# Kernel tuning notes

Hardware: AMD Instinct MI355X
Metric: run time of the kernel (lower is better)

The kernel has to match this reference:

```python
import jax, jax.numpy as jnp
import numpy as np

EPS = 1e-5  # torch LayerNorm default


def _ln(x, w, b):
    m = jnp.mean(x, axis=-1, keepdims=True)
    v = jnp.mean((x - m) ** 2, axis=-1, keepdims=True)
    return (x - m) / jnp.sqrt(v + EPS) * w + b


def _conv1x1(x, w, b):
    # x: [B,C,H,W], w: [O,C], b: [O]
    return jnp.einsum('bchw,oc->bohw', x, w) + b[None, :, None, None]


def setup_inputs() -> dict:
    key = jax.random.key(0)
    ks = jax.random.split(key, 5)
    B, Cin, H, W = 8, 384, 64, 64
    D, N = 128, 512
    s = lambda k, shape, scale=0.02: jax.random.normal(k, shape, jnp.float32) * scale
    return {
        'x': jax.random.normal(ks[0], (B, Cin, H, W), jnp.float32),
        'DR': jax.random.normal(ks[1], (N, D), jnp.float32),
        'conv_in_w': s(ks[2], (D, Cin)),
        'conv_in_b': jnp.zeros((D,), jnp.float32),
        'sem_w': s(ks[3], (D, D)),
        'sem_b': jnp.zeros((D,), jnp.float32),
        'norm1_w': jnp.ones((D,), jnp.float32),
        'norm1_b': jnp.zeros((D,), jnp.float32),
        'norm2_w': jnp.ones((D,), jnp.float32),
        'norm2_b': jnp.zeros((D,), jnp.float32),
        'conv_out_w': s(ks[4], (Cin, D)),
        'conv_out_b': jnp.zeros((Cin,), jnp.float32),
    }


def reference(x, DR, conv_in_w, conv_in_b, sem_w, sem_b, norm1_w, norm1_b,
              norm2_w, norm2_b, conv_out_w, conv_out_b):
    B, _, H, W = x.shape
    N = DR.shape[0]
    x_align = _conv1x1(x, conv_in_w, conv_in_b)                      # [B,D,H,W]
    x_sem = _conv1x1(x_align, sem_w, sem_b)                          # semantic_extra (1x1 conv)
    x_sem = x_sem.transpose(0, 2, 3, 1).reshape(B, H * W, -1)        # [B,HW,D]
    x_sem = _ln(x_sem, norm1_w, norm1_b)
    dr = _ln(DR, norm2_w, norm2_b).T                                 # [D,N] (same for all batches)
    # NOTE: original applies norm_1 TWICE for the numerator (faithful quirk)
    c_u = jnp.einsum('bld,dn->bln', _ln(x_sem, norm1_w, norm1_b), dr)  # [B,HW,N]
    c_d_l = jnp.sqrt(jnp.sum(x_sem ** 2, axis=-1, keepdims=True))      # [B,HW,1]
    c_d_r = jnp.sqrt(jnp.sum(dr ** 2, axis=0, keepdims=True))[None]    # [1,1,N]
    sim = c_u / (c_d_l * c_d_r)
    sim_soft = jax.nn.softmax(sim, axis=-1)                          # [B,HW,N]
    sim2d = sim_soft.transpose(0, 2, 1).reshape(B, N, H, W)
    degrad = jnp.einsum('bln,dn->bdl', sim_soft, dr).reshape(B, -1, H, W)  # [B,D,H,W]
    # pow-mask with per-batch min-max normalization
    mask_v = jnp.max(sim2d ** 3, axis=1, keepdims=True)              # [B,1,H,W]
    mn = jnp.min(mask_v.reshape(B, -1), axis=1).reshape(B, 1, 1, 1)
    mx = jnp.max(mask_v.reshape(B, -1), axis=1).reshape(B, 1, 1, 1)
    mask_v = 1.0 - (mask_v - mn) / (mx - mn)
    # topk row selection (torch fancy indexing gives [B,B,K,N]; squeeze(1) is a no-op for B>1)
    max_values = jnp.max(sim_soft, axis=2)                           # [B,HW]
    K = (H * W) // 50
    _, top_idx = jax.lax.top_k(max_values, K)                        # [B,K]
    results = jnp.take(sim_soft, top_idx, axis=1)                    # [B,B,K,N]
    out_img = _conv1x1(degrad, conv_out_w, conv_out_b)               # [B,Cin,H,W]
    return (mask_v, out_img, results)
```

## Files before the change

### kernel.cpp

```cpp
#include <hip/hip_runtime.h>
#include <cstdint>

#define EPS 1e-5f
#define BB   8
#define CIN  384
#define HWs  4096
#define LT   32768
#define DD   128
#define NN   512
#define TOPK 81

typedef short short8 __attribute__((ext_vector_type(8)));
typedef float f32x4  __attribute__((ext_vector_type(4)));

__device__ __forceinline__ unsigned short f2bf(float x) {
  unsigned u = __float_as_uint(x);
  u += 0x7fffu + ((u >> 16) & 1u);
  return (unsigned short)(u >> 16);
}
__device__ __forceinline__ float bf2f(unsigned u16) {
  return __uint_as_float(u16 << 16);
}
__device__ __forceinline__ void put_frag(unsigned short* buf, int tile, int rc, int k, float v) {
  int ks = k >> 5, g = (k >> 3) & 3, j = k & 7;
  int basehw = ((tile * 4 + ks) * 2) * 512 + (g * 16 + rc) * 8 + j;
  unsigned short hi = f2bf(v);
  buf[basehw] = hi;
  buf[basehw + 512] = f2bf(v - bf2f(hi));
}

__global__ __launch_bounds__(64) void k_dr(const float* __restrict__ DR,
    const float* __restrict__ w2, const float* __restrict__ b2,
    const float* __restrict__ w1, const float* __restrict__ b1,
    unsigned short* __restrict__ drwF, unsigned short* __restrict__ drlnF,
    float* __restrict__ t2, float* __restrict__ rcr) {
  int n = blockIdx.x;
  int lane = threadIdx.x;
  const float* row = DR + n * DD;
  float x0 = row[lane], x1 = row[lane + 64];
  float s = x0 + x1, sq = x0 * x0 + x1 * x1;
  #pragma unroll
  for (int o = 32; o; o >>= 1) { s += __shfl_xor(s, o); sq += __shfl_xor(sq, o); }
  float m = s * (1.f / 128.f);
  float v = sq * (1.f / 128.f) - m * m;
  float inv = rsqrtf(v + EPS);
  float y0 = (x0 - m) * inv * w2[lane] + b2[lane];
  float y1 = (x1 - m) * inv * w2[lane + 64] + b2[lane + 64];
  int nt = n >> 4, cc = n & 15;
  put_frag(drwF, nt, cc, lane, y0 * w1[lane]);
  put_frag(drwF, nt, cc, lane + 64, y1 * w1[lane + 64]);
  int ks = n >> 5, gB = (n >> 3) & 3, j = n & 7;
  {
    int d = lane;
    unsigned short hi = f2bf(y0);
    int base = (((d >> 4) * 16 + ks) * 2) * 512 + (gB * 16 + (d & 15)) * 8 + j;
    drlnF[base] = hi;
    drlnF[base + 512] = f2bf(y0 - bf2f(hi));
  }
  {
    int d = lane + 64;
    unsigned short hi = f2bf(y1);
    int base = (((d >> 4) * 16 + ks) * 2) * 512 + (gB * 16 + (d & 15)) * 8 + j;
    drlnF[base] = hi;
    drlnF[base + 512] = f2bf(y1 - bf2f(hi));
  }
  float pt2 = y0 * b1[lane] + y1 * b1[lane + 64];
  float pss = y0 * y0 + y1 * y1;
  #pragma unroll
  for (int o = 32; o; o >>= 1) { pt2 += __shfl_xor(pt2, o); pss += __shfl_xor(pss, o); }
  if (lane == 0) { t2[n] = pt2; rcr[n] = rsqrtf(pss); }
}

__global__ __launch_bounds__(256) void k_bprep(const float* __restrict__ src,
                                               unsigned short* __restrict__ dst,
                                               int K) {
  int rt = blockIdx.x, kb = blockIdx.y;
  int t = threadIdx.x, m = t >> 4, kg = t & 15;
  int k0 = kb * 128 + kg * 8;
  const float* s = src + (size_t)(rt * 16 + m) * K + k0;
  float4 f0 = *(const float4*)s;
  float4 f1 = *(const float4*)(s + 4);
  float vs[8] = {f0.x, f0.y, f0.z, f0.w, f1.x, f1.y, f1.z, f1.w};
  short8 hi, lo;
  #pragma unroll
  for (int j = 0; j < 8; ++j) {
    unsigned short h = f2bf(vs[j]);
    hi[j] = (short)h;
    lo[j] = (short)f2bf(vs[j] - bf2f(h));
  }
  int nkt = K >> 5;
  int ks = k0 >> 5, g = (k0 >> 3) & 3;
  short8* D8 = (short8*)dst;
  int base = ((rt * nkt + ks) * 2) * 64 + g * 16 + m;
  D8[base] = hi;
  D8[base + 64] = lo;
}

__global__ __launch_bounds__(256) void k_convsem(const float* __restrict__ x,
    const unsigned short* __restrict__ WinF, const float* __restrict__ bin,
    const unsigned short* __restrict__ semWF, const float* __restrict__ sb,
    const float* __restrict__ w1, const float* __restrict__ b1,
    unsigned short* __restrict__ ApF, float* __restrict__ rclv) {
  __shared__ unsigned int shbuf[32 * 132];
  __shared__ float sredS[32][4], sredQ[32][4];
  __shared__ float rowM[32], rowI[32];
  int t = threadIdx.x;
  int w = t >> 6, lane = t & 63, m = lane & 15, g = lane >> 4;
  int l0 = blockIdx.x * 32;
  int b = l0 >> 12, hw0 = l0 & 4095;
  const float* xb = x + (size_t)b * CIN * HWs + hw0;
  const short8* B8 = (const short8*)WinF;
  int chs = t & 31, hwo = (t >> 5) * 4;
  const float* xs = xb + (size_t)chs * HWs + hwo;
  f32x4 acc[2][2];
  #pragma unroll
  for (int lt = 0; lt < 2; ++lt)
    #pragma unroll
    for (int j2 = 0; j2 < 2; ++j2) acc[lt][j2] = (f32x4){0.f, 0.f, 0.f, 0.f};
  float4 u = *(const float4*)xs;
  for (int ks = 0; ks < 12; ++ks) {
    {
      float vv[4] = {u.x, u.y, u.z, u.w};
      #pragma unroll
      for (int i = 0; i < 4; ++i) {
        unsigned short h = f2bf(vv[i]);
        unsigned short lo = f2bf(vv[i] - bf2f(h));
        shbuf[(hwo + i) * 36 + chs] = (unsigned)h | ((unsigned)lo << 16);
      }
    }
    __syncthreads();
    if (ks < 11) u = *(const float4*)(xs + (size_t)((ks + 1) * 32) * HWs);
    short8 ah[2], al[2];
    #pragma unroll
    for (int lt = 0; lt < 2; ++lt) {
      const unsigned* src = &shbuf[(lt * 16 + m) * 36 + g * 8];
      uint4 p0 = *(const uint4*)(src);
      uint4 p1 = *(const uint4*)(src + 4);
      unsigned uu[8] = {p0.x, p0.y, p0.z, p0.w, p1.x, p1.y, p1.z, p1.w};
      unsigned* ahp = (unsigned*)&ah[lt];
      unsigned* alp = (unsigned*)&al[lt];
      #pragma unroll
      for (int jj = 0; jj < 4; ++jj) {
        unsigned e0 = uu[2 * jj], e1 = uu[2 * jj + 1];
        ahp[jj] = (e0 & 0xffffu) | (e1 << 16);
        alp[jj] = (e0 >> 16) | (e1 & 0xffff0000u);
      }
    }
    #pragma unroll
    for (int j2 = 0; j2 < 2; ++j2) {
      int dt = w * 2 + j2;
      short8 bh = B8[((dt * 12 + ks) * 2 + 0) * 64 + lane];
      short8 bl = B8[((dt * 12 + ks) * 2 + 1) * 64 + lane];
      #pragma unroll
      for (int lt = 0; lt < 2; ++lt) {
        acc[lt][j2] = __builtin_amdgcn_mfma_f32_16x16x32_bf16(ah[lt], bh, acc[lt][j2], 0, 0, 0);
        acc[lt][j2] = __builtin_amdgcn_mfma_f32_16x16x32_bf16(ah[lt], bl, acc[lt][j2], 0, 0, 0);
        acc[lt][j2] = __builtin_amdgcn_mfma_f32_16x16x32_bf16(al[lt], bh, acc[lt][j2], 0, 0, 0);
      }
    }
    __syncthreads();
  }
  {
    float bia[2] = {bin[w * 32 + m], bin[w * 32 + 16 + m]};
    #pragma unroll
    for (int lt = 0; lt < 2; ++lt)
      #pragma unroll
      for (int j2 = 0; j2 < 2; ++j2)
        #pragma unroll
        for (int r = 0; r < 4; ++r) {
          float v = acc[lt][j2][r] + bia[j2];
          unsigned short h = f2bf(v);
          unsigned short lo = f2bf(v - bf2f(h));
          shbuf[(lt * 16 + g * 4 + r) * 132 + (w * 2 + j2) * 16 + m] =
              (unsigned)h | ((unsigned)lo << 16);
        }
  }
  __syncthreads();
  const short8* S8 = (const short8*)semWF;
  f32x4 acc2[2][2];
  #pragma unroll
  for (int lt = 0; lt < 2; ++lt)
    #pragma unroll
    for (int j2 = 0; j2 < 2; ++j2) acc2[lt][j2] = (f32x4){0.f, 0.f, 0.f, 0.f};
  #pragma unroll
  for (int ks2 = 0; ks2 < 4; ++ks2) {
    short8 ah2[2], al2[2];
    #pragma unroll
    for (int lt = 0; lt < 2; ++lt) {
      const unsigned* src = &shbuf[(lt * 16 + m) * 132 + ks2 * 32 + g * 8];
      uint4 p0 = *(const uint4*)(src);
      uint4 p1 = *(const uint4*)(src + 4);
      unsigned uu[8] = {p0.x, p0.y, p0.z, p0.w, p1.x, p1.y, p1.z, p1.w};
      unsigned* ahp = (unsigned*)&ah2[lt];
      unsigned* alp = (unsigned*)&al2[lt];
      #pragma unroll
      for (int jj = 0; jj < 4; ++jj) {
        unsigned e0 = uu[2 * jj], e1 = uu[2 * jj + 1];
        ahp[jj] = (e0 & 0xffffu) | (e1 << 16);
        alp[jj] = (e0 >> 16) | (e1 & 0xffff0000u);
      }
    }
    #pragma unroll
    for (int j2 = 0; j2 < 2; ++j2) {
      int dt = w * 2 + j2;
      short8 bh = S8[((dt * 4 + ks2) * 2 + 0) * 64 + lane];
      short8 bl = S8[((dt * 4 + ks2) * 2 + 1) * 64 + lane];
      #pragma unroll
      for (int lt = 0; lt < 2; ++lt) {
        acc2[lt][j2] = __builtin_amdgcn_mfma_f32_16x16x32_bf16(ah2[lt], bh, acc2[lt][j2], 0, 0, 0);
        acc2[lt][j2] = __builtin_amdgcn_mfma_f32_16x16x32_bf16(ah2[lt], bl, acc2[lt][j2], 0, 0, 0);
        acc2[lt][j2] = __builtin_amdgcn_mfma_f32_16x16x32_bf16(al2[lt], bh, acc2[lt][j2], 0, 0, 0);
      }
    }
  }
  {
    float bia2[2] = {sb[w * 32 + m], sb[w * 32 + 16 + m]};
    #pragma unroll
    for (int lt = 0; lt < 2; ++lt)
      #pragma unroll
      for (int j2 = 0; j2 < 2; ++j2)
        #pragma unroll
        for (int r = 0; r < 4; ++r) acc2[lt][j2][r] += bia2[j2];
  }
  float s1[2][4], q1[2][4];
  #pragma unroll
  for (int lt = 0; lt < 2; ++lt)
    #pragma unroll
    for (int r = 0; r < 4; ++r) {
      float a = acc2[lt][0][r], b2v = acc2[lt][1][r];
      s1[lt][r] = a + b2v;
      q1[lt][r] = a * a + b2v * b2v;
    }
  #pragma unroll
  for (int o = 1; o < 16; o <<= 1)
    #pragma unroll
    for (int lt = 0; lt < 2; ++lt)
      #pragma unroll
      for (int r = 0; r < 4; ++r) {
        s1[lt][r] += __shfl_xor(s1[lt][r], o);
        q1[lt][r] += __shfl_xor(q1[lt][r], o);
      }
  if (m == 0) {
    #pragma unroll
    for (int lt = 0; lt < 2; ++lt)
      #pragma unroll
      for (int r = 0; r < 4; ++r) {
        sredS[lt * 16 + g * 4 + r][w] = s1[lt][r];
        sredQ[lt * 16 + g * 4 + r][w] = q1[lt][r];
      }
  }
  __syncthreads();
  if (t < 32) {
    float S = sredS[t][0] + sredS[t][1] + sredS[t][2] + sredS[t][3];
    float Q = sredQ[t][0] + sredQ[t][1] + sredQ[t][2] + sredQ[t][3];
    float mu = S * (1.f / 128.f);
    float var = Q * (1.f / 128.f) - mu * mu;
    rowM[t] = mu;
    rowI[t] = rsqrtf(var + EPS);
  }
  __syncthreads();
  float w1v[2] = {w1[w * 32 + m], w1[w * 32 + 16 + m]};
  float b1v[2] = {b1[w * 32 + m], b1[w * 32 + 16 + m]};
  #pragma unroll
  for (int lt = 0; lt < 2; ++lt)
    #pragma unroll
    for (int r = 0; r < 4; ++r) {
      float mu = rowM[lt * 16 + g * 4 + r];
      float iv = rowI[lt * 16 + g * 4 + r];
      float y0 = (acc2[lt][0][r] - mu) * iv * w1v[0] + b1v[0];
      float y1 = (acc2[lt][1][r] - mu) * iv * w1v[1] + b1v[1];
      acc2[lt][0][r] = y0; acc2[lt][1][r] = y1;
      s1[lt][r] = y0 + y1;
      q1[lt][r] = y0 * y0 + y1 * y1;
    }
  #pragma unroll
  for (int o = 1; o < 16; o <<= 1)
    #pragma unroll
    for (int lt = 0; lt < 2; ++lt)
      #pragma unroll
      for (int r = 0; r < 4; ++r) {
        s1[lt][r] += __shfl_xor(s1[lt][r], o);
        q1[lt][r] += __shfl_xor(q1[lt][r], o);
      }
  if (m == 0) {
    #pragma unroll
    for (int lt = 0; lt < 2; ++lt)
      #pragma unroll
      for (int r = 0; r < 4; ++r) {
        sredS[lt * 16 + g * 4 + r][w] = s1[lt][r];
        sredQ[lt * 16 + g * 4 + r][w] = q1[lt][r];
      }
  }
  __syncthreads();
  if (t < 32) {
    float S = sredS[t][0] + sredS[t][1] + sredS[t][2] + sredS[t][3];
    float Q = sredQ[t][0] + sredQ[t][1] + sredQ[t][2] + sredQ[t][3];
    float m2 = S * (1.f / 128.f);
    float v2 = Q * (1.f / 128.f) - m2 * m2;
    float inv2 = rsqrtf(v2 + EPS);
    float rcl = rsqrtf(Q);
    rowM[t] = m2;
    rowI[t] = inv2 * rcl;
    rclv[l0 + t] = rcl;
  }
  __syncthreads();
  float* smemf = (float*)shbuf;
  #pragma unroll
  for (int lt = 0; lt < 2; ++lt)
    #pragma unroll
    for (int r = 0; r < 4; ++r) {
      float m2 = rowM[lt * 16 + g * 4 + r];
      float sc = rowI[lt * 16 + g * 4 + r];
      smemf[(lt * 16 + g * 4 + r) * 132 + w * 32 + m] = (acc2[lt][0][r] - m2) * sc;
      smemf[(lt * 16 + g * 4 + r) * 132 + w * 32 + 16 + m] = (acc2[lt][1][r] - m2) * sc;
    }
  __syncthreads();
  short8* O8 = (short8*)ApF;
  #pragma unroll
  for (int it = 0; it < 2; ++it) {
    int idx = it * 256 + t;
    int l = idx & 31, dq = idx >> 5;
    const float* src = &smemf[l * 132 + dq * 8];
    float4 f0 = *(const float4*)src;
    float4 f1 = *(const float4*)(src + 4);
    float vs[8] = {f0.x, f0.y, f0.z, f0.w, f1.x, f1.y, f1.z, f1.w};
    short8 hi, lo;
    #pragma unroll
    for (int j = 0; j < 8; ++j) {
      unsigned short h = f2bf(vs[j]);
      hi[j] = (short)h;
      lo[j] = (short)f2bf(vs[j] - bf2f(h));
    }
    int ltg = (l0 + l) >> 4;
    int idx8 = ((ltg * 4 + (dq >> 2)) * 2) * 64 + (dq & 3) * 16 + (l & 15);
    O8[idx8] = hi;
    O8[idx8 + 64] = lo;
  }
}

__global__ __launch_bounds__(256) void k_scores(const unsigned short* __restrict__ ApF,
    const unsigned short* __restrict__ drwF, const float* __restrict__ t2g,
    const float* __restrict__ rcrg, const float* __restrict__ rclg,
    unsigned short* __restrict__ pF, float* __restrict__ maxv) {
  __shared__ __align__(16) float sredM[32][4];
  __shared__ __align__(16) float sredS[32][4];
  __shared__ __align__(16) unsigned short plds[32 * 520];
  int t = threadIdx.x;
  int w = t >> 6, lane = t & 63, c = lane & 15, g = lane >> 4;
  int l0 = blockIdx.x * 32;
  int lt0 = blockIdx.x * 2;
  const short8* A8 = (const short8*)ApF;
  const short8* B8 = (const short8*)drwF;
  f32x4 acc[2][8];
  #pragma unroll
  for (int il = 0; il < 2; ++il)
    #pragma unroll
    for (int jn = 0; jn < 8; ++jn) acc[il][jn] = (f32x4){0.f, 0.f, 0.f, 0.f};
  #pragma unroll
  for (int ks = 0; ks < 4; ++ks) {
    short8 ah0 = A8[((lt0 * 4 + ks) * 2 + 0) * 64 + lane];
    short8 al0 = A8[((lt0 * 4 + ks) * 2 + 1) * 64 + lane];
    short8 ah1 = A8[(((lt0 + 1) * 4 + ks) * 2 + 0) * 64 + lane];
    short8 al1 = A8[(((lt0 + 1) * 4 + ks) * 2 + 1) * 64 + lane];
    #pragma unroll
    for (int jn = 0; jn < 8; ++jn) {
      int nt = w * 8 + jn;
      short8 bh = B8[((nt * 4 + ks) * 2 + 0) * 64 + lane];
      short8 bl = B8[((nt * 4 + ks) * 2 + 1) * 64 + lane];
      acc[0][jn] = __builtin_amdgcn_mfma_f32_16x16x32_bf16(ah0, bh, acc[0][jn], 0, 0, 0);
      acc[0][jn] = __builtin_amdgcn_mfma_f32_16x16x32_bf16(ah0, bl, acc[0][jn], 0, 0, 0);
      acc[0][jn] = __builtin_amdgcn_mfma_f32_16x16x32_bf16(al0, bh, acc[0][jn], 0, 0, 0);
      acc[1][jn] = __builtin_amdgcn_mfma_f32_16x16x32_bf16(ah1, bh, acc[1][jn], 0, 0, 0);
      acc[1][jn] = __builtin_amdgcn_mfma_f32_16x16x32_bf16(ah1, bl, acc[1][jn], 0, 0, 0);
      acc[1][jn] = __builtin_amdgcn_mfma_f32_16x16x32_bf16(al1, bh, acc[1][jn], 0, 0, 0);
    }
  }
  float rcrv[8], t2v[8];
  #pragma unroll
  for (int jn = 0; jn < 8; ++jn) {
    int n = w * 128 + jn * 16 + c;
    rcrv[jn] = rcrg[n]; t2v[jn] = t2g[n];
  }
  float rclr[2][4];
  #pragma unroll
  for (int il = 0; il < 2; ++il)
    #pragma unroll
    for (int r = 0; r < 4; ++r)
      rclr[il][r] = rclg[l0 + il * 16 + g * 4 + r];
  float M[2][4];
  #pragma unroll
  for (int il = 0; il < 2; ++il)
    #pragma unroll
    for (int r = 0; r < 4; ++r) M[il][r] = -1e30f;
  #pragma unroll
  for (int il = 0; il < 2; ++il)
    #pragma unroll
    for (int jn = 0; jn < 8; ++jn) {
      f32x4 a = acc[il][jn];
      #pragma unroll
      for (int r = 0; r < 4; ++r) {
        float s = rcrv[jn] * (a[r] + rclr[il][r] * t2v[jn]);
        a[r] = s;
        M[il][r] = fmaxf(M[il][r], s);
      }
      acc[il][jn] = a;
    }
  #pragma unroll
  for (int o = 1; o < 16; o <<= 1)
    #pragma unroll
    for (int il = 0; il < 2; ++il)
      #pragma unroll
      for (int r = 0; r < 4; ++r)
        M[il][r] = fmaxf(M[il][r], __shfl_xor(M[il][r], o));
  if (c == 0) {
    #pragma unroll
    for (int il = 0; il < 2; ++il)
      #pragma unroll
      for (int r = 0; r < 4; ++r)
        sredM[il * 16 + g * 4 + r][w] = M[il][r];
  }
  __syncthreads();
  float Mf[2][4];
  #pragma unroll
  for (int il = 0; il < 2; ++il)
    #pragma unroll
    for (int r = 0; r < 4; ++r) {
      f32x4 mv = *(const f32x4*)(&sredM[il * 16 + g * 4 + r][0]);
      Mf[il][r] = fmaxf(fmaxf(mv[0], mv[1]), fmaxf(mv[2], mv[3]));
    }
  float S[2][4];
  #pragma unroll
  for (int il = 0; il < 2; ++il)
    #pragma unroll
    for (int r = 0; r < 4; ++r) S[il][r] = 0.f;
  #pragma unroll
  for (int il = 0; il < 2; ++il)
    #pragma unroll
    for (int jn = 0; jn < 8; ++jn) {
      f32x4 a = acc[il][jn];
      #pragma unroll
      for (int r = 0; r < 4; ++r) {
        float e = __expf(a[r] - Mf[il][r]);
        a[r] = e;
        S[il][r] += e;
      }
      acc[il][jn] = a;
    }
  #pragma unroll
  for (int o = 1; o < 16; o <<= 1)
    #pragma unroll
    for (int il = 0; il < 2; ++il)
      #pragma unroll
      for (int r = 0; r < 4; ++r)
        S[il][r] += __shfl_xor(S[il][r], o);
  if (c == 0) {
    #pragma unroll
    for (int il = 0; il < 2; ++il)
      #pragma unroll
      for (int r = 0; r < 4; ++r)
        sredS[il * 16 + g * 4 + r][w] = S[il][r];
  }
  __syncthreads();
  float RS[2][4];
  #pragma unroll
  for (int il = 0; il < 2; ++il)
    #pragma unroll
    for (int r = 0; r < 4; ++r) {
      f32x4 sv = *(const f32x4*)(&sredS[il * 16 + g * 4 + r][0]);
      float tot = sv[0] + sv[1] + sv[2] + sv[3];
      RS[il][r] = 1.f / tot;
    }
  if (w == 0 && c == 0) {
    #pragma unroll
    for (int il = 0; il < 2; ++il)
      #pragma unroll
      for (int r = 0; r < 4; ++r)
        maxv[l0 + il * 16 + g * 4 + r] = RS[il][r];
  }
  #pragma unroll
  for (int il = 0; il < 2; ++il)
    #pragma unroll
    for (int jn = 0; jn < 8; ++jn)
      #pragma unroll
      for (int r = 0; r < 4; ++r)
        plds[(il * 16 + g * 4 + r) * 520 + w * 128 + jn * 16 + c] =
            f2bf(acc[il][jn][r] * RS[il][r]);
  __syncthreads();
  short8* P8o = (short8*)pF;
  #pragma unroll
  for (int it = 0; it < 8; ++it) {
    int slot = it * 256 + t;
    int ltl = slot >> 10;
    int ks = (slot >> 6) & 15;
    int gB = (slot >> 4) & 3;
    int mrow = slot & 15;
    int row = ltl * 16 + mrow;
    int n0 = ks * 32 + gB * 8;
    short8 v = *(const short8*)(&plds[row * 520 + n0]);
    P8o[blockIdx.x * 2048 + slot] = v;
  }
}

__global__ __launch_bounds__(256) void k_deg(const unsigned short* __restrict__ pF,
    const unsigned short* __restrict__ drlnF, const unsigned short* __restrict__ WoF,
    const float* __restrict__ bo, float* __restrict__ out_img) {
  __shared__ float smem[64 * 132];
  int t = threadIdx.x;
  int w = t >> 6, lane = t & 63, c = lane & 15, g = lane >> 4;
  int l0 = blockIdx.x * 64;
  int lt0 = l0 >> 4;
  const short8* P8 = (const short8*)pF;
  const short8* D8 = (const short8*)drlnF;
  const short8* W8 = (const short8*)WoF;
  f32x4 acc[4][2];
  #pragma unroll
  for (int lt = 0; lt < 4; ++lt)
    #pragma unroll
    for (int j2 = 0; j2 < 2; ++j2) acc[lt][j2] = (f32x4){0.f, 0.f, 0.f, 0.f};
  for (int ks = 0; ks < 16; ++ks) {
    short8 a0 = P8[((lt0 + 0) * 16 + ks) * 64 + lane];
    short8 a1 = P8[((lt0 + 1) * 16 + ks) * 64 + lane];
    short8 a2 = P8[((lt0 + 2) * 16 + ks) * 64 + lane];
    short8 a3 = P8[((lt0 + 3) * 16 + ks) * 64 + lane];
    #pragma unroll
    for (int j2 = 0; j2 < 2; ++j2) {
      int dt = w * 2 + j2;
      short8 bh = D8[((dt * 16 + ks) * 2 + 0) * 64 + lane];
      short8 bl = D8[((dt * 16 + ks) * 2 + 1) * 64 + lane];
      acc[0][j2] = __builtin_amdgcn_mfma_f32_16x16x32_bf16(a0, bh, acc[0][j2], 0, 0, 0);
      acc[0][j2] = __builtin_amdgcn_mfma_f32_16x16x32_bf16(a0, bl, acc[0][j2], 0, 0, 0);
      acc[1][j2] = __builtin_amdgcn_mfma_f32_16x16x32_bf16(a1, bh, acc[1][j2], 0, 0, 0);
      acc[1][j2] = __builtin_amdgcn_mfma_f32_16x16x32_bf16(a1, bl, acc[1][j2], 0, 0, 0);
      acc[2][j2] = __builtin_amdgcn_mfma_f32_16x16x32_bf16(a2, bh, acc[2][j2], 0, 0, 0);
      acc[2][j2] = __builtin_amdgcn_mfma_f32_16x16x32_bf16(a2, bl, acc[2][j2], 0, 0, 0);
      acc[3][j2] = __builtin_amdgcn_mfma_f32_16x16x32_bf16(a3, bh, acc[3][j2], 0, 0, 0);
      acc[3][j2] = __builtin_amdgcn_mfma_f32_16x16x32_bf16(a3, bl, acc[3][j2], 0, 0, 0);
    }
  }
  #pragma unroll
  for (int lt = 0; lt < 4; ++lt)
    #pragma unroll
    for (int j2 = 0; j2 < 2; ++j2)
      #pragma unroll
      for (int r = 0; r < 4; ++r)
        smem[(lt * 16 + g * 4 + r) * 132 + w * 32 + j2 * 16 + c] = acc[lt][j2][r];
  __syncthreads();
  f32x4 acc2[4][6];
  #pragma unroll
  for (int lt = 0; lt < 4; ++lt)
    #pragma unroll
    for (int ot = 0; ot < 6; ++ot) acc2[lt][ot] = (f32x4){0.f, 0.f, 0.f, 0.f};
  #pragma unroll
  for (int ks2 = 0; ks2 < 4; ++ks2) {
    short8 dh[4];
    #pragma unroll
    for (int lt = 0; lt < 4; ++lt) {
      const float* src = &smem[(lt * 16 + c) * 132 + ks2 * 32 + g * 8];
      float4 f0 = *(const float4*)src;
      float4 f1 = *(const float4*)(src + 4);
      float vs[8] = {f0.x, f0.y, f0.z, f0.w, f1.x, f1.y, f1.z, f1.w};
      #pragma unroll
      for (int j = 0; j < 8; ++j) dh[lt][j] = (short)f2bf(vs[j]);
    }
    #pragma unroll
    for (int ot = 0; ot < 6; ++ot) {
      int otg = w * 6 + ot;
      short8 wh = W8[((otg * 4 + ks2) * 2 + 0) * 64 + lane];
      short8 wl = W8[((otg * 4 + ks2) * 2 + 1) * 64 + lane];
      #pragma unroll
      for (int lt = 0; lt < 4; ++lt) {
        acc2[lt][ot] = __builtin_amdgcn_mfma_f32_16x16x32_bf16(dh[lt], wh, acc2[lt][ot], 0, 0, 0);
        acc2[lt][ot] = __builtin_amdgcn_mfma_f32_16x16x32_bf16(dh[lt], wl, acc2[lt][ot], 0, 0, 0);
      }
    }
  }
  __syncthreads();
  int b = l0 >> 12, hw0 = l0 & 4095;
  float* ob = out_img + (size_t)b * CIN * HWs + hw0;
  float bov[6];
  #pragma unroll
  for (int ot = 0; ot < 6; ++ot) bov[ot] = bo[w * 96 + ot * 16 + c];
  for (int ot = 0; ot < 6; ++ot) {
    #pragma unroll
    for (int lt = 0; lt < 4; ++lt)
      #pragma unroll
      for (int r = 0; r < 4; ++r)
        smem[(lt * 16 + g * 4 + r) * 65 + w * 16 + c] = acc2[lt][ot][r] + bov[ot];
    __syncthreads();
    #pragma unroll
    for (int i = 0; i < 16; ++i) {
      int idx = t + i * 256;
      int o_l = idx >> 6, ll = idx & 63;
      int o = (o_l >> 4) * 96 + ot * 16 + (o_l & 15);
      ob[(size_t)o * HWs + ll] = smem[ll * 65 + o_l];
    }
    __syncthreads();
  }
}

__global__ __launch_bounds__(256) void k_mask(const float* __restrict__ maxv,
                                              float* __restrict__ outm) {
  int b = blockIdx.x, t = threadIdx.x;
  float c[16];
  float mn = 1e30f, mx = -1e30f;
  #pragma unroll
  for (int j = 0; j < 16; ++j) {
    float x = maxv[b * HWs + t + j * 256];
    float cc = x * x * x;
    c[j] = cc;
    mn = fminf(mn, cc); mx = fmaxf(mx, cc);
  }
  #pragma unroll
  for (int o = 32; o; o >>= 1) { mn = fminf(mn, __shfl_xor(mn, o)); mx = fmaxf(mx, __shfl_xor(mx, o)); }
  __shared__ float smn[4], smx[4];
  int w = t >> 6;
  if ((t & 63) == 0) { smn[w] = mn; smx[w] = mx; }
  __syncthreads();
  mn = fminf(fminf(smn[0], smn[1]), fminf(smn[2], smn[3]));
  mx = fmaxf(fmaxf(smx[0], smx[1]), fmaxf(smx[2], smx[3]));
  float sc = 1.f / (mx - mn);
  #pragma unroll
  for (int j = 0; j < 16; ++j)
    outm[b * HWs + t + j * 256] = 1.f - (c[j] - mn) * sc;
}

__global__ __launch_bounds__(256) void k_topk(const float* __restrict__ maxv,
                                              int* __restrict__ tix) {
  __shared__ unsigned int hist[4][256];
  __shared__ unsigned long long slist[TOPK];
  __shared__ unsigned long long bc_prefix;
  __shared__ int bc_need, scount;
  int b = blockIdx.x, t = threadIdx.x;
  int w = t >> 6;
  unsigned long long key[16];
  #pragma unroll
  for (int j = 0; j < 16; ++j) {
    int idx = t + j * 256;
    unsigned int bits = __float_as_uint(maxv[b * HWs + idx]);
    key[j] = ((unsigned long long)bits << 12) | (unsigned)(4095 - idx);
  }
  if (t == 0) { bc_prefix = 0ull; bc_need = TOPK; scount = 0; }
  for (int r = 0; r < 6; ++r) {
    int shift = 40 - 8 * r;
    unsigned int* hflat = (unsigned int*)hist;
    hflat[t] = 0; hflat[t + 256] = 0; hflat[t + 512] = 0; hflat[t + 768] = 0;
    __syncthreads();
    unsigned long long prefix = bc_prefix;
    int bins[16];
    #pragma unroll
    for (int j = 0; j < 16; ++j)
      bins[j] = ((key[j] >> (shift + 8)) == prefix) ? (int)((key[j] >> shift) & 255) : -1;
    #pragma unroll
    for (int j = 0; j < 16; ++j) {
      if (bins[j] >= 0) {
        int cnt = 1;
        #pragma unroll
        for (int j2 = j + 1; j2 < 16; ++j2)
          if (bins[j2] == bins[j]) { bins[j2] = -1; ++cnt; }
        atomicAdd(&hist[w][bins[j]], (unsigned)cnt);
      }
    }
    __syncthreads();
    if (t < 64) {
      int cb[4], s = 0;
      #pragma unroll
      for (int j = 0; j < 4; ++j) {
        int bin = 255 - (t * 4 + j);
        cb[j] = (int)(hist[0][bin] + hist[1][bin] + hist[2][bin] + hist[3][bin]);
        s += cb[j];
      }
      int P = s;
      #pragma unroll
      for (int o = 1; o < 64; o <<= 1) {
        int u = __shfl_up(P, o);
        if (t >= o) P += u;
      }
      int need = bc_need;
      unsigned long long mask = __ballot(P >= need);
      int first = __ffsll((long long)mask) - 1;
      if (t == first) {
        int acc = P - s;
        #pragma unroll
        for (int j = 0; j < 4; ++j) {
          if (acc + cb[j] >= need) {
            bc_prefix = (prefix << 8) | (unsigned)(255 - (t * 4 + j));
            bc_need = need - acc;
            break;
          }
          acc += cb[j];
        }
      }
    }
    __syncthreads();
  }
  unsigned long long K81 = bc_prefix;
  #pragma unroll
  for (int j = 0; j < 16; ++j)
    if (key[j] >= K81) {
      int pos = atomicAdd(&scount, 1);
      slist[pos] = key[j];
    }
  __syncthreads();
  if (t < TOPK) {
    unsigned long long mine = slist[t];
    int rank = 0;
    for (int i = 0; i < TOPK; ++i) rank += (slist[i] > mine) ? 1 : 0;
    tix[b * TOPK + rank] = 4095 - (int)(mine & 0xFFFull);
  }
}

__global__ __launch_bounds__(128) void k_gather(const unsigned short* __restrict__ pF,
    const int* __restrict__ tix, float* __restrict__ outr) {
  int gB_ = blockIdx.x;
  int k = gB_ % TOPK;
  int bb = gB_ / TOPK;
  int b2 = bb & 7, b = bb >> 3;
  int l = b * HWs + tix[b2 * TOPK + k];
  int lt = l >> 4, mrow = l & 15;
  int t = threadIdx.x;
  int ks = t >> 3, gq = (t >> 1) & 3, j0 = (t & 1) * 4;
  int base = ((lt * 16 + ks) * 64 + gq * 16 + mrow) * 8 + j0;
  const unsigned* src = (const unsigned*)(pF + base);
  unsigned u0 = src[0], u1 = src[1];
  float4 v = {bf2f(u0 & 0xffffu), bf2f(u0 >> 16), bf2f(u1 & 0xffffu), bf2f(u1 >> 16)};
  *(float4*)(outr + (size_t)gB_ * NN + t * 4) = v;
}

extern "C" void kernel_launch(void* const* d_in, const int* in_sizes, int n_in,
                              void* d_out, int out_size, void* d_ws, size_t ws_size,
                              hipStream_t stream) {
  const float* x    = (const float*)d_in[0];
  const float* DR   = (const float*)d_in[1];
  const float* win  = (const float*)d_in[2];
  const float* bin  = (const float*)d_in[3];
  const float* sw   = (const float*)d_in[4];
  const float* sb   = (const float*)d_in[5];
  const float* n1w  = (const float*)d_in[6];
  const float* n1b  = (const float*)d_in[7];
  const float* n2w  = (const float*)d_in[8];
  const float* n2b  = (const float*)d_in[9];
  const float* wout = (const float*)d_in[10];
  const float* bout = (const float*)d_in[11];
  float* out = (float*)d_out;
  float* W = (float*)d_ws;

  unsigned short* drwF  = (unsigned short*)(W);
  float* t2   = W + 65536;
  float* rcr  = W + 66048;
  float* rclv = W + 66560;
  float* maxv = W + 99328;
  unsigned short* drlnF = (unsigned short*)(W + 132096);
  unsigned short* WoF   = (unsigned short*)(W + 197632);
  unsigned short* WinF  = (unsigned short*)(W + 246784);
  unsigned short* semWF = (unsigned short*)(W + 295936);
  unsigned short* ApF   = (unsigned short*)(W + 312320);
  unsigned short* pF    = (unsigned short*)(W + 4506624);
  int*   tix  = (int*)(W + 12895232);

  float* out_mask = out;
  float* out_img  = out + 32768;
  float* out_res  = out + 32768 + 12582912;

  k_dr     <<<NN, 64, 0, stream>>>(DR, n2w, n2b, n1w, n1b, drwF, drlnF, t2, rcr);
  k_bprep  <<<dim3(8, 3),  256, 0, stream>>>(win,  WinF,  CIN);
  k_bprep  <<<dim3(8, 1),  256, 0, stream>>>(sw,   semWF, DD);
  k_bprep  <<<dim3(24, 1), 256, 0, stream>>>(wout, WoF,   DD);
  k_convsem<<<1024, 256, 0, stream>>>(x, WinF, bin, semWF, sb, n1w, n1b, ApF, rclv);
  k_scores <<<1024, 256, 0, stream>>>(ApF, drwF, t2, rcr, rclv, pF, maxv);
  k_deg    <<<512,  256, 0, stream>>>(pF, drlnF, WoF, bout, out_img);
  k_mask   <<<BB,   256, 0, stream>>>(maxv, out_mask);
  k_topk   <<<BB,   256, 0, stream>>>(maxv, tix);
  k_gather <<<BB * BB * TOPK, 128, 0, stream>>>(pF, tix, out_res);
}
```

Before: 225.9 us.

## Prefetch all conv_in input channels upfront and batch LDS stages to cut barriers

The conv_in stage of k_convsem now issues all twelve global float4 loads at the start, so every load is in flight at once instead of one step ahead. It splits the hi/lo bf16 input into two halves of six k-slices each, held in a larger shared buffer, which cuts the barrier count from twenty-four to four. A launch-bounds occupancy hint of four blocks per CU is also added. The risk is higher register pressure from holding forty-eight floats per thread. The bigger LDS footprint (about 27KB) could limit occupancy or clash with the later stages that reuse shbuf with a 132 stride.

After: 226.5 us. About the same (+0.3%).

```diff
diff --git a/kernel.cpp b/kernel.cpp
--- a/kernel.cpp
+++ b/kernel.cpp
@@ -96,12 +96,12 @@
   D8[base + 64] = lo;
 }
 
-__global__ __launch_bounds__(256) void k_convsem(const float* __restrict__ x,
+__global__ __launch_bounds__(256, 4) void k_convsem(const float* __restrict__ x,
     const unsigned short* __restrict__ WinF, const float* __restrict__ bin,
     const unsigned short* __restrict__ semWF, const float* __restrict__ sb,
     const float* __restrict__ w1, const float* __restrict__ b1,
     unsigned short* __restrict__ ApF, float* __restrict__ rclv) {
-  __shared__ unsigned int shbuf[32 * 132];
+  __shared__ unsigned int shbuf[6 * 32 * 36];
   __shared__ float sredS[32][4], sredQ[32][4];
   __shared__ float rowM[32], rowI[32];
   int t = threadIdx.x;
@@ -112,50 +112,59 @@
   const short8* B8 = (const short8*)WinF;
   int chs = t & 31, hwo = (t >> 5) * 4;
   const float* xs = xb + (size_t)chs * HWs + hwo;
+  float4 xu[12];
+  #pragma unroll
+  for (int ks = 0; ks < 12; ++ks)
+    xu[ks] = *(const float4*)(xs + (size_t)(ks * 32) * HWs);
   f32x4 acc[2][2];
   #pragma unroll
   for (int lt = 0; lt < 2; ++lt)
     #pragma unroll
     for (int j2 = 0; j2 < 2; ++j2) acc[lt][j2] = (f32x4){0.f, 0.f, 0.f, 0.f};
-  float4 u = *(const float4*)xs;
-  for (int ks = 0; ks < 12; ++ks) {
-    {
-      float vv[4] = {u.x, u.y, u.z, u.w};
-      #pragma unroll
-      for (int i = 0; i < 4; ++i) {
-        unsigned short h = f2bf(vv[i]);
-        unsigned short lo = f2bf(vv[i] - bf2f(h));
-        shbuf[(hwo + i) * 36 + chs] = (unsigned)h | ((unsigned)lo << 16);
+  #pragma unroll
+  for (int h = 0; h < 2; ++h) {
+    #pragma unroll
+    for (int i = 0; i < 6; ++i) {
+      float4 uv = xu[h * 6 + i];
+      float vv[4] = {uv.x, uv.y, uv.z, uv.w};
+      #pragma unroll
+      for (int jj = 0; jj < 4; ++jj) {
+        unsigned short hh = f2bf(vv[jj]);
+        unsigned short lo = f2bf(vv[jj] - bf2f(hh));
+        shbuf[i * 1152 + (hwo + jj) * 36 + chs] = (unsigned)hh | ((unsigned)lo << 16);
       }
     }
     __syncthreads();
-    if (ks < 11) u = *(const float4*)(xs + (size_t)((ks + 1) * 32) * HWs);
-    short8 ah[2], al[2];
-    #pragma unroll
-    for (int lt = 0; lt < 2; ++lt) {
-      const unsigned* src = &shbuf[(lt * 16 + m) * 36 + g * 8];
-      uint4 p0 = *(const uint4*)(src);
-      uint4 p1 = *(const uint4*)(src + 4);
-      unsigned uu[8] = {p0.x, p0.y, p0.z, p0.w, p1.x, p1.y, p1.z, p1.w};
-      unsigned* ahp = (unsigned*)&ah[lt];
-      unsigned* alp = (unsigned*)&al[lt];
-      #pragma unroll
-      for (int jj = 0; jj < 4; ++jj) {
-        unsigned e0 = uu[2 * jj], e1 = uu[2 * jj + 1];
-        ahp[jj] = (e0 & 0xffffu) | (e1 << 16);
-        alp[jj] = (e0 >> 16) | (e1 & 0xffff0000u);
-      }
-    }
-    #pragma unroll
-    for (int j2 = 0; j2 < 2; ++j2) {
-      int dt = w * 2 + j2;
-      short8 bh = B8[((dt * 12 + ks) * 2 + 0) * 64 + lane];
-      short8 bl = B8[((dt * 12 + ks) * 2 + 1) * 64 + lane];
+    #pragma unroll
+    for (int i = 0; i < 6; ++i) {
+      int ks = h * 6 + i;
+      short8 ah[2], al[2];
       #pragma unroll
       for (int lt = 0; lt < 2; ++lt) {
-        acc[lt][j2] = __builtin_amdgcn_mfma_f32_16x16x32_bf16(ah[lt], bh, acc[lt][j2], 0, 0, 0);
-        acc[lt][j2] = __builtin_amdgcn_mfma_f32_16x16x32_bf16(ah[lt], bl, acc[lt][j2], 0, 0, 0);
-        acc[lt][j2] = __builtin_amdgcn_mfma_f32_16x16x32_bf16(al[lt], bh, acc[lt][j2], 0, 0, 0);
+        const unsigned* src = &shbuf[i * 1152 + (lt * 16 + m) * 36 + g * 8];
+        uint4 p0 = *(const uint4*)(src);
+        uint4 p1 = *(const uint4*)(src + 4);
+        unsigned uu[8] = {p0.x, p0.y, p0.z, p0.w, p1.x, p1.y, p1.z, p1.w};
+        unsigned* ahp = (unsigned*)&ah[lt];
+        unsigned* alp = (unsigned*)&al[lt];
+        #pragma unroll
+        for (int jj = 0; jj < 4; ++jj) {
+          unsigned e0 = uu[2 * jj], e1 = uu[2 * jj + 1];
+          ahp[jj] = (e0 & 0xffffu) | (e1 << 16);
+          alp[jj] = (e0 >> 16) | (e1 & 0xffff0000u);
+        }
+      }
+      #pragma unroll
+      for (int j2 = 0; j2 < 2; ++j2) {
+        int dt = w * 2 + j2;
+        short8 bh = B8[((dt * 12 + ks) * 2 + 0) * 64 + lane];
+        short8 bl = B8[((dt * 12 + ks) * 2 + 1) * 64 + lane];
+        #pragma unroll
+        for (int lt = 0; lt < 2; ++lt) {
+          acc[lt][j2] = __builtin_amdgcn_mfma_f32_16x16x32_bf16(ah[lt], bh, acc[lt][j2], 0, 0, 0);
+          acc[lt][j2] = __builtin_amdgcn_mfma_f32_16x16x32_bf16(ah[lt], bl, acc[lt][j2], 0, 0, 0);
+          acc[lt][j2] = __builtin_amdgcn_mfma_f32_16x16x32_bf16(al[lt], bh, acc[lt][j2], 0, 0, 0);
+        }
       }
     }
     __syncthreads();
```

## Load whole x tile into LDS upfront and drop per-k-step barriers in convsem

Applied to the files above, without the earlier changes.

The conv_in stage now issues all twelve channel-slab loads of the 32-pixel x tile at once into a 384x33 fp32 LDS array, then runs the MFMA loop without the two per-iteration __syncthreads. The bf16 hi/lo split moves from the store side into the per-fragment read from LDS. LDS use per block grows to about 50KB and the kernel is given a min-blocks hint of 3. The intent is more memory-level parallelism and fewer barriers, at the cost of repeated conversion work and possibly lower occupancy or register pressure.

Result: no change. 227.4 us (+0.7%).

```diff
diff --git a/kernel.cpp b/kernel.cpp
--- a/kernel.cpp
+++ b/kernel.cpp
@@ -96,54 +96,47 @@
   D8[base + 64] = lo;
 }
 
-__global__ __launch_bounds__(256) void k_convsem(const float* __restrict__ x,
+__global__ __launch_bounds__(256, 3) void k_convsem(const float* __restrict__ x,
     const unsigned short* __restrict__ WinF, const float* __restrict__ bin,
     const unsigned short* __restrict__ semWF, const float* __restrict__ sb,
     const float* __restrict__ w1, const float* __restrict__ b1,
     unsigned short* __restrict__ ApF, float* __restrict__ rclv) {
-  __shared__ unsigned int shbuf[32 * 132];
+  __shared__ float xt[CIN * 33];
   __shared__ float sredS[32][4], sredQ[32][4];
   __shared__ float rowM[32], rowI[32];
   int t = threadIdx.x;
   int w = t >> 6, lane = t & 63, m = lane & 15, g = lane >> 4;
   int l0 = blockIdx.x * 32;
   int b = l0 >> 12, hw0 = l0 & 4095;
-  const float* xb = x + (size_t)b * CIN * HWs + hw0;
+  {
+    const float* xs = x + (size_t)b * CIN * HWs + (size_t)(t >> 3) * HWs + hw0 + (t & 7) * 4;
+    float4 v[12];
+    #pragma unroll
+    for (int r = 0; r < 12; ++r)
+      v[r] = *(const float4*)(xs + (size_t)(r * 32) * HWs);
+    #pragma unroll
+    for (int r = 0; r < 12; ++r) {
+      float* d = &xt[(r * 32 + (t >> 3)) * 33 + (t & 7) * 4];
+      d[0] = v[r].x; d[1] = v[r].y; d[2] = v[r].z; d[3] = v[r].w;
+    }
+  }
+  __syncthreads();
   const short8* B8 = (const short8*)WinF;
-  int chs = t & 31, hwo = (t >> 5) * 4;
-  const float* xs = xb + (size_t)chs * HWs + hwo;
   f32x4 acc[2][2];
   #pragma unroll
   for (int lt = 0; lt < 2; ++lt)
     #pragma unroll
     for (int j2 = 0; j2 < 2; ++j2) acc[lt][j2] = (f32x4){0.f, 0.f, 0.f, 0.f};
-  float4 u = *(const float4*)xs;
   for (int ks = 0; ks < 12; ++ks) {
-    {
-      float vv[4] = {u.x, u.y, u.z, u.w};
-      #pragma unroll
-      for (int i = 0; i < 4; ++i) {
-        unsigned short h = f2bf(vv[i]);
-        unsigned short lo = f2bf(vv[i] - bf2f(h));
-        shbuf[(hwo + i) * 36 + chs] = (unsigned)h | ((unsigned)lo << 16);
-      }
-    }
-    __syncthreads();
-    if (ks < 11) u = *(const float4*)(xs + (size_t)((ks + 1) * 32) * HWs);
     short8 ah[2], al[2];
     #pragma unroll
     for (int lt = 0; lt < 2; ++lt) {
-      const unsigned* src = &shbuf[(lt * 16 + m) * 36 + g * 8];
-      uint4 p0 = *(const uint4*)(src);
-      uint4 p1 = *(const uint4*)(src + 4);
-      unsigned uu[8] = {p0.x, p0.y, p0.z, p0.w, p1.x, p1.y, p1.z, p1.w};
-      unsigned* ahp = (unsigned*)&ah[lt];
-      unsigned* alp = (unsigned*)&al[lt];
-      #pragma unroll
-      for (int jj = 0; jj < 4; ++jj) {
-        unsigned e0 = uu[2 * jj], e1 = uu[2 * jj + 1];
-        ahp[jj] = (e0 & 0xffffu) | (e1 << 16);
-        alp[jj] = (e0 >> 16) | (e1 & 0xffff0000u);
+      #pragma unroll
+      for (int j = 0; j < 8; ++j) {
+        float xv = xt[(ks * 32 + g * 8 + j) * 33 + lt * 16 + m];
+        unsigned short h = f2bf(xv);
+        ah[lt][j] = (short)h;
+        al[lt][j] = (short)f2bf(xv - bf2f(h));
       }
     }
     #pragma unroll
@@ -158,8 +151,9 @@
         acc[lt][j2] = __builtin_amdgcn_mfma_f32_16x16x32_bf16(al[lt], bh, acc[lt][j2], 0, 0, 0);
       }
     }
-    __syncthreads();
-  }
+  }
+  __syncthreads();
+  unsigned int* plane = (unsigned int*)xt;
   {
     float bia[2] = {bin[w * 32 + m], bin[w * 32 + 16 + m]};
     #pragma unroll
@@ -171,7 +165,7 @@
           float v = acc[lt][j2][r] + bia[j2];
           unsigned short h = f2bf(v);
           unsigned short lo = f2bf(v - bf2f(h));
-          shbuf[(lt * 16 + g * 4 + r) * 132 + (w * 2 + j2) * 16 + m] =
+          plane[(lt * 16 + g * 4 + r) * 132 + (w * 2 + j2) * 16 + m] =
               (unsigned)h | ((unsigned)lo << 16);
         }
   }
@@ -187,7 +181,7 @@
     short8 ah2[2], al2[2];
     #pragma unroll
     for (int lt = 0; lt < 2; ++lt) {
-      const unsigned* src = &shbuf[(lt * 16 + m) * 132 + ks2 * 32 + g * 8];
+      const unsigned* src = &plane[(lt * 16 + m) * 132 + ks2 * 32 + g * 8];
       uint4 p0 = *(const uint4*)(src);
       uint4 p1 = *(const uint4*)(src + 4);
       unsigned uu[8] = {p0.x, p0.y, p0.z, p0.w, p1.x, p1.y, p1.z, p1.w};
@@ -304,15 +298,15 @@
     rclv[l0 + t] = rcl;
   }
   __syncthreads();
-  float* smemf = (float*)shbuf;
+  float* planef = (float*)xt;
   #pragma unroll
   for (int lt = 0; lt < 2; ++lt)
     #pragma unroll
     for (int r = 0; r < 4; ++r) {
       float m2 = rowM[lt * 16 + g * 4 + r];
       float sc = rowI[lt * 16 + g * 4 + r];
-      smemf[(lt * 16 + g * 4 + r) * 132 + w * 32 + m] = (acc2[lt][0][r] - m2) * sc;
-      smemf[(lt * 16 + g * 4 + r) * 132 + w * 32 + 16 + m] = (acc2[lt][1][r] - m2) * sc;
+      planef[(lt * 16 + g * 4 + r) * 132 + w * 32 + m] = (acc2[lt][0][r] - m2) * sc;
+      planef[(lt * 16 + g * 4 + r) * 132 + w * 32 + 16 + m] = (acc2[lt][1][r] - m2) * sc;
     }
   __syncthreads();
   short8* O8 = (short8*)ApF;
@@ -320,7 +314,7 @@
   for (int it = 0; it < 2; ++it) {
     int idx = it * 256 + t;
     int l = idx & 31, dq = idx >> 5;
-    const float* src = &smemf[l * 132 + dq * 8];
+    const float* src = &planef[l * 132 + dq * 8];
     float4 f0 = *(const float4*)src;
     float4 f1 = *(const float4*)(src + 4);
     float vs[8] = {f0.x, f0.y, f0.z, f0.w, f1.x, f1.y, f1.z, f1.w};
```
